# Performance work log

Measured on AMD Instinct MI355X. Metric: run time of the kernel, lower is better.

The kernel has to match this reference:

```python
import jax, jax.numpy as jnp
import numpy as np

DIM = 1024
NUM_HEADS = 8
HEAD_DIM = 64
INNER = NUM_HEADS * HEAD_DIM  # 512


def setup_inputs() -> dict:
    key = jax.random.key(0)
    ks = jax.random.split(key, 7)
    B, N, M = 8, 512, 4096
    x = jax.random.normal(ks[0], (B, N, DIM), dtype=jnp.float32)
    context = jax.random.normal(ks[1], (B, M, DIM), dtype=jnp.float32)
    s_in = 1.0 / np.sqrt(DIM)
    s_inner = 1.0 / np.sqrt(INNER)
    # Linear weights stored as [in, out] for x @ W
    Wq = jax.random.normal(ks[2], (DIM, INNER), dtype=jnp.float32) * s_in
    Wk = jax.random.normal(ks[3], (DIM, INNER), dtype=jnp.float32) * s_in
    Wv = jax.random.normal(ks[4], (DIM, INNER), dtype=jnp.float32) * s_in
    Wo = jax.random.normal(ks[5], (INNER, DIM), dtype=jnp.float32) * s_inner
    bo = jax.random.normal(ks[6], (DIM,), dtype=jnp.float32) * 0.01
    return {"x": x, "context": context, "Wq": Wq, "Wk": Wk, "Wv": Wv, "Wo": Wo, "bo": bo}


def reference(x, context, Wq, Wk, Wv, Wo, bo):
    B, N, _ = x.shape
    M = context.shape[1]
    scale = HEAD_DIM ** -0.5
    # project and split heads: [B, H, N, D]
    q = (x @ Wq).reshape(B, N, NUM_HEADS, HEAD_DIM).transpose(0, 2, 1, 3)
    k = (context @ Wk).reshape(B, M, NUM_HEADS, HEAD_DIM).transpose(0, 2, 1, 3)
    v = (context @ Wv).reshape(B, M, NUM_HEADS, HEAD_DIM).transpose(0, 2, 1, 3)
    # full attention matrix [B, H, N, M] as in the original module
    attn = jax.nn.softmax(jnp.einsum('bhnd,bhmd->bhnm', q, k) * scale, axis=-1)
    out = jnp.einsum('bhnm,bhmd->bhnd', attn, v)  # [B, H, N, D]
    out = out.transpose(0, 2, 1, 3).reshape(B, N, INNER)
    return out @ Wo + bo
```

## Files before the change

kernel.cpp:

```cpp
#include <hip/hip_runtime.h>
#include <hip/hip_bf16.h>

#define B_SZ 8
#define N_Q 512
#define M_KV 4096
#define DIM 1024
#define INNER 512
#define NHEADS 8
#define HDIM 64

typedef __attribute__((ext_vector_type(4))) float floatx4;
typedef __attribute__((ext_vector_type(8))) short shortx8;
typedef __attribute__((ext_vector_type(4))) short shortx4;

__device__ inline unsigned short f2bf(float f) {
  union { float f; unsigned u; } x; x.f = f;
  unsigned r = x.u + 0x7FFFu + ((x.u >> 16) & 1u);
  return (unsigned short)(r >> 16);
}

__global__ void k_transpose_bf16(const float* __restrict__ W,
                                 unsigned short* __restrict__ Wt,
                                 int K, int N) {
  int idx = blockIdx.x * 256 + threadIdx.x;
  if (idx >= K * N) return;
  int n = idx / K, k = idx - n * K;
  Wt[idx] = f2bf(W[(long)k * N + n]);
}

template<int MODE, bool ABF, int NCOL, int MBITS>
__global__ __launch_bounds__(256, 3)
void k_gemm(const void* __restrict__ Ap, const unsigned short* __restrict__ Bt,
            void* __restrict__ Cout, void* __restrict__ Cout2,
            const float* __restrict__ bias, int M, int N, int K, float oscale) {
  __shared__ unsigned short As[128][40];
  __shared__ unsigned short Bs[128][40];
  const int tid = threadIdx.x;
  const int lane = tid & 63;
  const int w = tid >> 6;
  const int wr = w >> 1, wc = w & 1;

  const int cpx = gridDim.x >> 3;
  const int L = (blockIdx.x & 7) * cpx + (blockIdx.x >> 3);
  const long arow0 = (long)(L / NCOL) * 128;
  const long bcol0 = (long)(L % NCOL) * 128;

  floatx4 acc[4][4] = {};

  const int ar = tid >> 3;
  const int ac = (tid & 7) * 4;
  const int hr = tid >> 1;
  const int hseg = (tid & 1) * 16;
  const float* Af = (const float*)Ap;
  const unsigned short* Ah = (const unsigned short*)Ap;

  if (ABF) {
    const unsigned short* src = Ah + (arow0 + hr) * K + hseg;
    *reinterpret_cast<shortx8*>(&As[hr][hseg]) =
        *reinterpret_cast<const shortx8*>(src);
    *reinterpret_cast<shortx8*>(&As[hr][hseg + 8]) =
        *reinterpret_cast<const shortx8*>(src + 8);
  } else {
    #pragma unroll
    for (int i = 0; i < 4; ++i) {
      int r = ar + i * 32;
      floatx4 v = *reinterpret_cast<const floatx4*>(Af + (arow0 + r) * K + ac);
      shortx4 h;
      h[0] = (short)f2bf(v[0]); h[1] = (short)f2bf(v[1]);
      h[2] = (short)f2bf(v[2]); h[3] = (short)f2bf(v[3]);
      *reinterpret_cast<shortx4*>(&As[r][ac]) = h;
    }
  }
  {
    const unsigned short* src = Bt + (bcol0 + hr) * K + hseg;
    *reinterpret_cast<shortx8*>(&Bs[hr][hseg]) =
        *reinterpret_cast<const shortx8*>(src);
    *reinterpret_cast<shortx8*>(&Bs[hr][hseg + 8]) =
        *reinterpret_cast<const shortx8*>(src + 8);
  }
  __syncthreads();

  for (int kt = 0; kt < K; kt += 32) {
    const bool has_next = (kt + 32) < K;
    floatx4 pAf[4];
    shortx8 pAh[2], pB[2];
    if (has_next) {
      if (ABF) {
        const unsigned short* src = Ah + (arow0 + hr) * K + kt + 32 + hseg;
        pAh[0] = *reinterpret_cast<const shortx8*>(src);
        pAh[1] = *reinterpret_cast<const shortx8*>(src + 8);
      } else {
        #pragma unroll
        for (int i = 0; i < 4; ++i)
          pAf[i] = *reinterpret_cast<const floatx4*>(
              Af + (arow0 + ar + i * 32) * K + kt + 32 + ac);
      }
      const unsigned short* src = Bt + (bcol0 + hr) * K + kt + 32 + hseg;
      pB[0] = *reinterpret_cast<const shortx8*>(src);
      pB[1] = *reinterpret_cast<const shortx8*>(src + 8);
    }

    shortx8 af[4], bf[4];
    #pragma unroll
    for (int rb = 0; rb < 4; ++rb)
      af[rb] = *reinterpret_cast<const shortx8*>(
          &As[wr * 64 + rb * 16 + (lane & 15)][(lane >> 4) * 8]);
    #pragma unroll
    for (int cb = 0; cb < 4; ++cb)
      bf[cb] = *reinterpret_cast<const shortx8*>(
          &Bs[wc * 64 + cb * 16 + (lane & 15)][(lane >> 4) * 8]);
    #pragma unroll
    for (int rb = 0; rb < 4; ++rb) {
      #pragma unroll
      for (int cb = 0; cb < 4; ++cb)
        acc[rb][cb] = __builtin_amdgcn_mfma_f32_16x16x32_bf16(
            af[rb], bf[cb], acc[rb][cb], 0, 0, 0);
    }
    __syncthreads();

    if (has_next) {
      if (ABF) {
        *reinterpret_cast<shortx8*>(&As[hr][hseg]) = pAh[0];
        *reinterpret_cast<shortx8*>(&As[hr][hseg + 8]) = pAh[1];
      } else {
        #pragma unroll
        for (int i = 0; i < 4; ++i) {
          shortx4 h;
          h[0] = (short)f2bf(pAf[i][0]); h[1] = (short)f2bf(pAf[i][1]);
          h[2] = (short)f2bf(pAf[i][2]); h[3] = (short)f2bf(pAf[i][3]);
          *reinterpret_cast<shortx4*>(&As[ar + i * 32][ac]) = h;
        }
      }
      *reinterpret_cast<shortx8*>(&Bs[hr][hseg]) = pB[0];
      *reinterpret_cast<shortx8*>(&Bs[hr][hseg + 8]) = pB[1];
      __syncthreads();
    }
  }

  #pragma unroll
  for (int rb = 0; rb < 4; ++rb) {
    #pragma unroll
    for (int cb = 0; cb < 4; ++cb) {
      long gr0 = arow0 + wr * 64 + rb * 16 + (lane >> 4) * 4;
      long gc  = bcol0 + wc * 64 + cb * 16 + (lane & 15);
      if (MODE == 0) {
        float bv = bias[gc];
        #pragma unroll
        for (int r = 0; r < 4; ++r)
          ((float*)Cout)[(gr0 + r) * N + gc] = acc[rb][cb][r] + bv;
      } else if (MODE == 2) {
        long b = gr0 >> MBITS, m = gr0 & ((1 << MBITS) - 1);
        long h = gc >> 6, d = gc & 63;
        #pragma unroll
        for (int r = 0; r < 4; ++r)
          ((unsigned short*)Cout)[((((b * 8 + h) << MBITS) + m + r) << 6) + d] =
              f2bf(acc[rb][cb][r] * oscale);
      } else {
        long b = gr0 >> 12, m = gr0 & 4095;
        if (gc < 512) {
          long h = gc >> 6, d = gc & 63;
          #pragma unroll
          for (int r = 0; r < 4; ++r)
            ((unsigned short*)Cout)[((((b * 8 + h) << 12) + m + r) << 6) + d] =
                f2bf(acc[rb][cb][r]);
        } else {
          long h = (gc - 512) >> 6, d = (gc - 512) & 63;
          shortx4 hv;
          #pragma unroll
          for (int r = 0; r < 4; ++r) hv[r] = (short)f2bf(acc[rb][cb][r]);
          *reinterpret_cast<shortx4*>(
              &((unsigned short*)Cout2)[(((b * 8 + h) * 64 + d) << 12) + m]) = hv;
        }
      }
    }
  }
}

__global__ __launch_bounds__(256, 2)
void k_attn(const unsigned short* __restrict__ Qh,
            const unsigned short* __restrict__ Kh,
            const unsigned short* __restrict__ Vt,
            unsigned short* __restrict__ Aout) {
  __shared__ unsigned short Ks[64][72];
  __shared__ unsigned short Vs[64][72];
  __shared__ unsigned short QPs[64][72];
  const int tid = threadIdx.x;
  const int lane = tid & 63;
  const int w = tid >> 6;
  const int wg = blockIdx.x;
  const int bh = wg & 63;
  const int qt = wg >> 6;
  const int b = bh >> 3, h = bh & 7;

  const unsigned short* Qbase = Qh + (((long)bh << 9) + qt * 64) * 64;
  const unsigned short* Kbase = Kh + (((long)bh) << 18);
  const unsigned short* Vbase = Vt + (((long)bh) << 18);

  const int sr = tid >> 2;
  const int sc = (tid & 3) * 16;

  {
    const unsigned short* src = Qbase + sr * 64 + sc;
    *reinterpret_cast<shortx8*>(&QPs[sr][sc]) =
        *reinterpret_cast<const shortx8*>(src);
    *reinterpret_cast<shortx8*>(&QPs[sr][sc + 8]) =
        *reinterpret_cast<const shortx8*>(src + 8);
  }
  {
    const unsigned short* ksrc = Kbase + sr * 64 + sc;
    *reinterpret_cast<shortx8*>(&Ks[sr][sc]) =
        *reinterpret_cast<const shortx8*>(ksrc);
    *reinterpret_cast<shortx8*>(&Ks[sr][sc + 8]) =
        *reinterpret_cast<const shortx8*>(ksrc + 8);
    const unsigned short* vsrc = Vbase + ((long)sr << 12) + sc;
    *reinterpret_cast<shortx8*>(&Vs[sr][sc]) =
        *reinterpret_cast<const shortx8*>(vsrc);
    *reinterpret_cast<shortx8*>(&Vs[sr][sc + 8]) =
        *reinterpret_cast<const shortx8*>(vsrc + 8);
  }
  __syncthreads();

  shortx8 qf[2];
  qf[0] = *reinterpret_cast<const shortx8*>(
      &QPs[w * 16 + (lane & 15)][(lane >> 4) * 8]);
  qf[1] = *reinterpret_cast<const shortx8*>(
      &QPs[w * 16 + (lane & 15)][32 + (lane >> 4) * 8]);

  floatx4 o_acc[4] = {};
  float l_part[4] = {0.f, 0.f, 0.f, 0.f};
  shortx8 kpre[2], vpre[2];

  for (int mt = 0; mt < M_KV / 64; ++mt) {
    if (mt < M_KV / 64 - 1) {
      const unsigned short* ksrc = Kbase + ((mt + 1) * 64 + sr) * 64 + sc;
      kpre[0] = *reinterpret_cast<const shortx8*>(ksrc);
      kpre[1] = *reinterpret_cast<const shortx8*>(ksrc + 8);
      const unsigned short* vsrc = Vbase + ((long)sr << 12) + (mt + 1) * 64 + sc;
      vpre[0] = *reinterpret_cast<const shortx8*>(vsrc);
      vpre[1] = *reinterpret_cast<const shortx8*>(vsrc + 8);
    }

    floatx4 s[4];
    #pragma unroll
    for (int cb = 0; cb < 4; ++cb) {
      shortx8 k0 = *reinterpret_cast<const shortx8*>(
          &Ks[cb * 16 + (lane & 15)][(lane >> 4) * 8]);
      shortx8 k1 = *reinterpret_cast<const shortx8*>(
          &Ks[cb * 16 + (lane & 15)][32 + (lane >> 4) * 8]);
      floatx4 z = {};
      z = __builtin_amdgcn_mfma_f32_16x16x32_bf16(qf[0], k0, z, 0, 0, 0);
      s[cb] = __builtin_amdgcn_mfma_f32_16x16x32_bf16(qf[1], k1, z, 0, 0, 0);
    }

    #pragma unroll
    for (int cb = 0; cb < 4; ++cb) {
      #pragma unroll
      for (int r = 0; r < 4; ++r) {
        float pv = __expf(s[cb][r]);
        l_part[r] += pv;
        QPs[w * 16 + (lane >> 4) * 4 + r][cb * 16 + (lane & 15)] = f2bf(pv);
      }
    }

    #pragma unroll
    for (int kk = 0; kk < 2; ++kk) {
      shortx8 pf = *reinterpret_cast<const shortx8*>(
          &QPs[w * 16 + (lane & 15)][kk * 32 + (lane >> 4) * 8]);
      #pragma unroll
      for (int db = 0; db < 4; ++db) {
        shortx8 vf = *reinterpret_cast<const shortx8*>(
            &Vs[db * 16 + (lane & 15)][kk * 32 + (lane >> 4) * 8]);
        o_acc[db] = __builtin_amdgcn_mfma_f32_16x16x32_bf16(
            pf, vf, o_acc[db], 0, 0, 0);
      }
    }

    __syncthreads();
    if (mt < M_KV / 64 - 1) {
      *reinterpret_cast<shortx8*>(&Ks[sr][sc]) = kpre[0];
      *reinterpret_cast<shortx8*>(&Ks[sr][sc + 8]) = kpre[1];
      *reinterpret_cast<shortx8*>(&Vs[sr][sc]) = vpre[0];
      *reinterpret_cast<shortx8*>(&Vs[sr][sc + 8]) = vpre[1];
      __syncthreads();
    }
  }

  float inv[4];
  #pragma unroll
  for (int r = 0; r < 4; ++r) {
    float l = l_part[r];
    l += __shfl_xor(l, 1);
    l += __shfl_xor(l, 2);
    l += __shfl_xor(l, 4);
    l += __shfl_xor(l, 8);
    inv[r] = 1.f / l;
  }
  #pragma unroll
  for (int db = 0; db < 4; ++db) {
    #pragma unroll
    for (int r = 0; r < 4; ++r) {
      int n = qt * 64 + w * 16 + (lane >> 4) * 4 + r;
      long idx = ((long)(b * N_Q + n)) * INNER + h * HDIM + db * 16 + (lane & 15);
      Aout[idx] = f2bf(o_acc[db][r] * inv[r]);
    }
  }
}

extern "C" void kernel_launch(void* const* d_in, const int* in_sizes, int n_in,
                              void* d_out, int out_size, void* d_ws, size_t ws_size,
                              hipStream_t stream) {
  const float* x   = (const float*)d_in[0];
  const float* ctx = (const float*)d_in[1];
  const float* Wq  = (const float*)d_in[2];
  const float* Wk  = (const float*)d_in[3];
  const float* Wv  = (const float*)d_in[4];
  const float* Wo  = (const float*)d_in[5];
  const float* bo  = (const float*)d_in[6];
  float* out = (float*)d_out;

  char* ws = (char*)d_ws;
  unsigned short* Qh   = (unsigned short*)(ws);
  unsigned short* Kh   = (unsigned short*)(ws + (4ull  << 20));
  unsigned short* Vt   = (unsigned short*)(ws + (36ull << 20));
  unsigned short* Aat  = (unsigned short*)(ws + (68ull << 20));
  unsigned short* Wqt  = (unsigned short*)(ws + (72ull << 20));
  unsigned short* Wkvt = (unsigned short*)(ws + (73ull << 20));
  unsigned short* Wot  = (unsigned short*)(ws + (75ull << 20));

  k_transpose_bf16<<<(DIM * INNER + 255) / 256, 256, 0, stream>>>(Wq, Wqt, DIM, INNER);
  k_transpose_bf16<<<(DIM * INNER + 255) / 256, 256, 0, stream>>>(Wk, Wkvt, DIM, INNER);
  k_transpose_bf16<<<(DIM * INNER + 255) / 256, 256, 0, stream>>>(
      Wv, Wkvt + (size_t)INNER * DIM, DIM, INNER);
  k_transpose_bf16<<<(INNER * DIM + 255) / 256, 256, 0, stream>>>(Wo, Wot, INNER, DIM);

  dim3 blk(256);
  k_gemm<2, false, 4, 9><<<dim3(4 * 32), blk, 0, stream>>>(
      x, Wqt, Qh, nullptr, nullptr, B_SZ * N_Q, INNER, DIM, 0.125f);
  k_gemm<4, false, 8, 12><<<dim3(8 * 256), blk, 0, stream>>>(
      ctx, Wkvt, Kh, Vt, nullptr, B_SZ * M_KV, 2 * INNER, DIM, 1.0f);

  k_attn<<<dim3(B_SZ * NHEADS * (N_Q / 64)), blk, 0, stream>>>(Qh, Kh, Vt, Aat);

  k_gemm<0, true, 8, 0><<<dim3(8 * 32), blk, 0, stream>>>(
      Aat, Wot, out, nullptr, bo, B_SZ * N_Q, DIM, INNER, 1.0f);
}
```

Baseline: 231.1 us.

## Use direct global-to-LDS loads with double-buffered swizzled tiles in GEMM

Rewrites the projection GEMM kernel to use 512-thread blocks computing 128x256 tiles. B (and bf16 A) tiles are loaded with global_load_lds straight into double-buffered, XOR-swizzled shared memory, and fp32 A is converted after the MFMA step. This is meant to drop the register round trip and one barrier per k-step, avoid LDS bank conflicts, and overlap loads with compute. The cost is fewer blocks in the grid (e.g. 64 for the Q projection), which may underfill the GPU, plus more LDS per block.

```diff
diff --git a/kernel.cpp b/kernel.cpp
--- a/kernel.cpp
+++ b/kernel.cpp
@@ -19,6 +19,12 @@
   return (unsigned short)(r >> 16);
 }
 
+__device__ inline void gload16(const void* g, void* l) {
+  __builtin_amdgcn_global_load_lds(
+      (const __attribute__((address_space(1))) void*)g,
+      (__attribute__((address_space(3))) void*)l, 16, 0, 0);
+}
+
 __global__ void k_transpose_bf16(const float* __restrict__ W,
                                  unsigned short* __restrict__ Wt,
                                  int K, int N) {
@@ -29,86 +35,91 @@
 }
 
 template<int MODE, bool ABF, int NCOL, int MBITS>
-__global__ __launch_bounds__(256, 3)
+__global__ __launch_bounds__(512, 4)
 void k_gemm(const void* __restrict__ Ap, const unsigned short* __restrict__ Bt,
             void* __restrict__ Cout, void* __restrict__ Cout2,
             const float* __restrict__ bias, int M, int N, int K, float oscale) {
-  __shared__ unsigned short As[128][40];
-  __shared__ unsigned short Bs[128][40];
+  __shared__ unsigned short As[2][128 * 32];
+  __shared__ unsigned short Bs[2][256 * 32];
   const int tid = threadIdx.x;
   const int lane = tid & 63;
   const int w = tid >> 6;
-  const int wr = w >> 1, wc = w & 1;
+  const int wr = w >> 2, wc = w & 3;
 
   const int cpx = gridDim.x >> 3;
   const int L = (blockIdx.x & 7) * cpx + (blockIdx.x >> 3);
   const long arow0 = (long)(L / NCOL) * 128;
-  const long bcol0 = (long)(L % NCOL) * 128;
-
-  floatx4 acc[4][4] = {};
-
-  const int ar = tid >> 3;
-  const int ac = (tid & 7) * 4;
-  const int hr = tid >> 1;
-  const int hseg = (tid & 1) * 16;
+  const long bcol0 = (long)(L % NCOL) * 256;
+
   const float* Af = (const float*)Ap;
   const unsigned short* Ah = (const unsigned short*)Ap;
 
+  const int lsub = lane >> 2;
+  const int lchunk = (lane & 3) ^ (lsub & 3);
+  const long brow0 = bcol0 + (w * 2 + 0) * 16 + lsub;
+  const long brow1 = bcol0 + (w * 2 + 1) * 16 + lsub;
+  const long ahrow = arow0 + w * 16 + lsub;
+  const int arow = tid >> 2;
+  const int acseg = tid & 3;
+  const int aswz = arow * 32 + ((acseg ^ (arow & 3)) * 8);
+
+  floatx4 acc[4][4] = {};
+
+  #define STAGE_B(buf, kt)                                                   \
+    {                                                                        \
+      gload16(Bt + brow0 * K + (kt) + lchunk * 8, &Bs[buf][(w * 2) * 512]);  \
+      gload16(Bt + brow1 * K + (kt) + lchunk * 8,                            \
+              &Bs[buf][(w * 2 + 1) * 512]);                                  \
+    }
+  #define STAGE_AH(buf, kt) \
+    gload16(Ah + ahrow * K + (kt) + lchunk * 8, &As[buf][w * 512]);
+
   if (ABF) {
-    const unsigned short* src = Ah + (arow0 + hr) * K + hseg;
-    *reinterpret_cast<shortx8*>(&As[hr][hseg]) =
-        *reinterpret_cast<const shortx8*>(src);
-    *reinterpret_cast<shortx8*>(&As[hr][hseg + 8]) =
-        *reinterpret_cast<const shortx8*>(src + 8);
+    STAGE_AH(0, 0);
   } else {
-    #pragma unroll
-    for (int i = 0; i < 4; ++i) {
-      int r = ar + i * 32;
-      floatx4 v = *reinterpret_cast<const floatx4*>(Af + (arow0 + r) * K + ac);
-      shortx4 h;
-      h[0] = (short)f2bf(v[0]); h[1] = (short)f2bf(v[1]);
-      h[2] = (short)f2bf(v[2]); h[3] = (short)f2bf(v[3]);
-      *reinterpret_cast<shortx4*>(&As[r][ac]) = h;
-    }
-  }
-  {
-    const unsigned short* src = Bt + (bcol0 + hr) * K + hseg;
-    *reinterpret_cast<shortx8*>(&Bs[hr][hseg]) =
-        *reinterpret_cast<const shortx8*>(src);
-    *reinterpret_cast<shortx8*>(&Bs[hr][hseg + 8]) =
-        *reinterpret_cast<const shortx8*>(src + 8);
-  }
+    const float* src = Af + (arow0 + arow) * (long)K + acseg * 8;
+    floatx4 a0 = *reinterpret_cast<const floatx4*>(src);
+    floatx4 a1 = *reinterpret_cast<const floatx4*>(src + 4);
+    shortx8 h;
+    h[0] = (short)f2bf(a0[0]); h[1] = (short)f2bf(a0[1]);
+    h[2] = (short)f2bf(a0[2]); h[3] = (short)f2bf(a0[3]);
+    h[4] = (short)f2bf(a1[0]); h[5] = (short)f2bf(a1[1]);
+    h[6] = (short)f2bf(a1[2]); h[7] = (short)f2bf(a1[3]);
+    *reinterpret_cast<shortx8*>(&As[0][aswz]) = h;
+  }
+  STAGE_B(0, 0);
   __syncthreads();
 
-  for (int kt = 0; kt < K; kt += 32) {
-    const bool has_next = (kt + 32) < K;
-    floatx4 pAf[4];
-    shortx8 pAh[2], pB[2];
-    if (has_next) {
+  const int NK = K >> 5;
+  for (int i = 0; i < NK; ++i) {
+    const int cur = i & 1;
+    const bool more = (i + 1) < NK;
+    floatx4 a0, a1;
+    if (more) {
+      const long ktn = (long)(i + 1) << 5;
+      STAGE_B(cur ^ 1, ktn);
       if (ABF) {
-        const unsigned short* src = Ah + (arow0 + hr) * K + kt + 32 + hseg;
-        pAh[0] = *reinterpret_cast<const shortx8*>(src);
-        pAh[1] = *reinterpret_cast<const shortx8*>(src + 8);
+        STAGE_AH(cur ^ 1, ktn);
       } else {
-        #pragma unroll
-        for (int i = 0; i < 4; ++i)
-          pAf[i] = *reinterpret_cast<const floatx4*>(
-              Af + (arow0 + ar + i * 32) * K + kt + 32 + ac);
+        const float* src = Af + (arow0 + arow) * (long)K + ktn + acseg * 8;
+        a0 = *reinterpret_cast<const floatx4*>(src);
+        a1 = *reinterpret_cast<const floatx4*>(src + 4);
       }
-      const unsigned short* src = Bt + (bcol0 + hr) * K + kt + 32 + hseg;
-      pB[0] = *reinterpret_cast<const shortx8*>(src);
-      pB[1] = *reinterpret_cast<const shortx8*>(src + 8);
     }
 
     shortx8 af[4], bf[4];
     #pragma unroll
-    for (int rb = 0; rb < 4; ++rb)
+    for (int rb = 0; rb < 4; ++rb) {
+      int row = wr * 64 + rb * 16 + (lane & 15);
       af[rb] = *reinterpret_cast<const shortx8*>(
-          &As[wr * 64 + rb * 16 + (lane & 15)][(lane >> 4) * 8]);
-    #pragma unroll
-    for (int cb = 0; cb < 4; ++cb)
+          &As[cur][row * 32 + (((lane >> 4) ^ (row & 3)) * 8)]);
+    }
+    #pragma unroll
+    for (int cb = 0; cb < 4; ++cb) {
+      int row = wc * 64 + cb * 16 + (lane & 15);
       bf[cb] = *reinterpret_cast<const shortx8*>(
-          &Bs[wc * 64 + cb * 16 + (lane & 15)][(lane >> 4) * 8]);
+          &Bs[cur][row * 32 + (((lane >> 4) ^ (row & 3)) * 8)]);
+    }
     #pragma unroll
     for (int rb = 0; rb < 4; ++rb) {
       #pragma unroll
@@ -116,26 +127,19 @@
         acc[rb][cb] = __builtin_amdgcn_mfma_f32_16x16x32_bf16(
             af[rb], bf[cb], acc[rb][cb], 0, 0, 0);
     }
+
+    if (more && !ABF) {
+      shortx8 h;
+      h[0] = (short)f2bf(a0[0]); h[1] = (short)f2bf(a0[1]);
+      h[2] = (short)f2bf(a0[2]); h[3] = (short)f2bf(a0[3]);
+      h[4] = (short)f2bf(a1[0]); h[5] = (short)f2bf(a1[1]);
+      h[6] = (short)f2bf(a1[2]); h[7] = (short)f2bf(a1[3]);
+      *reinterpret_cast<shortx8*>(&As[cur ^ 1][aswz]) = h;
+    }
     __syncthreads();
-
-    if (has_next) {
-      if (ABF) {
-        *reinterpret_cast<shortx8*>(&As[hr][hseg]) = pAh[0];
-        *reinterpret_cast<shortx8*>(&As[hr][hseg + 8]) = pAh[1];
-      } else {
-        #pragma unroll
-        for (int i = 0; i < 4; ++i) {
-          shortx4 h;
-          h[0] = (short)f2bf(pAf[i][0]); h[1] = (short)f2bf(pAf[i][1]);
-          h[2] = (short)f2bf(pAf[i][2]); h[3] = (short)f2bf(pAf[i][3]);
-          *reinterpret_cast<shortx4*>(&As[ar + i * 32][ac]) = h;
-        }
-      }
-      *reinterpret_cast<shortx8*>(&Bs[hr][hseg]) = pB[0];
-      *reinterpret_cast<shortx8*>(&Bs[hr][hseg + 8]) = pB[1];
-      __syncthreads();
-    }
-  }
+  }
+  #undef STAGE_B
+  #undef STAGE_AH
 
   #pragma unroll
   for (int rb = 0; rb < 4; ++rb) {
@@ -333,14 +337,14 @@
       Wv, Wkvt + (size_t)INNER * DIM, DIM, INNER);
   k_transpose_bf16<<<(INNER * DIM + 255) / 256, 256, 0, stream>>>(Wo, Wot, INNER, DIM);
 
-  dim3 blk(256);
-  k_gemm<2, false, 4, 9><<<dim3(4 * 32), blk, 0, stream>>>(
+  dim3 blk(512);
+  k_gemm<2, false, 2, 9><<<dim3(64), blk, 0, stream>>>(
       x, Wqt, Qh, nullptr, nullptr, B_SZ * N_Q, INNER, DIM, 0.125f);
-  k_gemm<4, false, 8, 12><<<dim3(8 * 256), blk, 0, stream>>>(
+  k_gemm<4, false, 4, 12><<<dim3(1024), blk, 0, stream>>>(
       ctx, Wkvt, Kh, Vt, nullptr, B_SZ * M_KV, 2 * INNER, DIM, 1.0f);
 
-  k_attn<<<dim3(B_SZ * NHEADS * (N_Q / 64)), blk, 0, stream>>>(Qh, Kh, Vt, Aat);
-
-  k_gemm<0, true, 8, 0><<<dim3(8 * 32), blk, 0, stream>>>(
+  k_attn<<<dim3(B_SZ * NHEADS * (N_Q / 64)), dim3(256), 0, stream>>>(Qh, Kh, Vt, Aat);
+
+  k_gemm<0, true, 4, 0><<<dim3(128), blk, 0, stream>>>(
       Aat, Wot, out, nullptr, bo, B_SZ * N_Q, DIM, INNER, 1.0f);
 }
```

Measured after the change: 230.7 us. No clear change (-0.2%).
